# Kernel optimization log

Hardware: AMD Instinct MI355X
Metric: run time of the kernel (lower is better)

The kernel has to match this reference:

```python
import jax, jax.numpy as jnp
import numpy as np

N = 50000
E = 800000
TEXT_VOCAB = 7000
ACTION_DIM = 64
MAX_POS = 5120
POS_DIM = 128   # edge encoder out_dim
NODE_DIM = 128  # text_out 64 + type_out 64
EDGE_DIM = 128
H1 = 256
OUT = 32
NEG_SLOPE = 0.2


def _pos_table():
    # sinusoidal table, [MAX_POS+1, POS_DIM]; even cols = cos, odd cols = sin
    positions = np.arange(0, MAX_POS + 1, dtype=np.float32)
    inv_freq = 1.0 / (10000.0 ** (np.arange(0.0, POS_DIM, 2.0, dtype=np.float32) / POS_DIM))
    si = np.outer(positions, inv_freq)
    tab = np.zeros((MAX_POS + 1, POS_DIM), dtype=np.float32)
    tab[:, 1::2] = np.sin(si)
    tab[:, 0::2] = np.cos(si)
    return jnp.asarray(tab)


def setup_inputs() -> dict:
    key = jax.random.key(0)
    ks = jax.random.split(key, 32)
    ri = jax.random.randint
    nrm = lambda k, s, scale=0.05: (jax.random.normal(k, s, dtype=jnp.float32) * scale)
    x = jnp.stack([ri(ks[0], (N,), 0, TEXT_VOCAB + 1, dtype=jnp.int32),
                   ri(ks[1], (N,), 0, 3, dtype=jnp.int32)], axis=-1)
    edge_index = ri(ks[2], (2, E), 0, N, dtype=jnp.int32)
    edge_attr = jnp.stack([ri(ks[3], (E,), 0, 3, dtype=jnp.int32),
                           ri(ks[4], (E,), 0, MAX_POS + 1, dtype=jnp.int32)], axis=-1)
    d = {
        "x": x, "edge_index": edge_index, "edge_attr": edge_attr,
        "text_emb": nrm(ks[5], (TEXT_VOCAB + 1, 64), 1.0),
        "type_emb": nrm(ks[6], (3, 64), 1.0),
        "flow_emb": nrm(ks[7], (3, EDGE_DIM), 1.0),
        "pos_table": _pos_table(),
        "pos_W": nrm(ks[8], (POS_DIM, POS_DIM)), "pos_b": nrm(ks[9], (POS_DIM,)),
        "c1_Wl": nrm(ks[10], (NODE_DIM, H1)), "c1_bl": nrm(ks[11], (H1,)),
        "c1_Wr": nrm(ks[12], (NODE_DIM, H1)), "c1_br": nrm(ks[13], (H1,)),
        "c1_We": nrm(ks[14], (EDGE_DIM, H1)), "c1_att": nrm(ks[15], (H1,)),
        "c1_bias": nrm(ks[16], (H1,)),
        "c2_Wl": nrm(ks[17], (H1, OUT)), "c2_bl": nrm(ks[18], (OUT,)),
        "c2_Wr": nrm(ks[19], (H1, OUT)), "c2_br": nrm(ks[20], (OUT,)),
        "c2_We": nrm(ks[21], (EDGE_DIM, OUT)), "c2_att": nrm(ks[22], (OUT,)),
        "c2_bias": nrm(ks[23], (OUT,)),
        "policy_W": nrm(ks[24], (OUT, ACTION_DIM), 0.2), "policy_b": nrm(ks[25], (ACTION_DIM,)),
    }
    return d


def gatv2(h, src, dst, ea, Wl, bl, Wr, br, We, att, bias, n):
    # PyG GATv2Conv, heads=1, add_self_loops=True, fill_value='mean'
    loop_attr = jnp.broadcast_to(ea.mean(0), (n, ea.shape[1]))
    s = jnp.concatenate([src, jnp.arange(n, dtype=src.dtype)])
    d = jnp.concatenate([dst, jnp.arange(n, dtype=dst.dtype)])
    ea_full = jnp.concatenate([ea, loop_attr], axis=0)
    xl = h @ Wl + bl  # messages (source side)
    xr = h @ Wr + br  # destination side
    m = xl[s] + xr[d] + ea_full @ We          # [E+n, F]
    e = jnp.where(m > 0, m, NEG_SLOPE * m) @ att  # per-edge logit [E+n]
    emax = jax.ops.segment_max(e, d, num_segments=n)
    a = jnp.exp(e - emax[d])
    denom = jax.ops.segment_sum(a, d, num_segments=n)
    alpha = a / denom[d]
    return jax.ops.segment_sum(alpha[:, None] * xl[s], d, num_segments=n) + bias


def reference(x, edge_index, edge_attr, text_emb, type_emb, flow_emb, pos_table,
              pos_W, pos_b,
              c1_Wl, c1_bl, c1_Wr, c1_br, c1_We, c1_att, c1_bias,
              c2_Wl, c2_bl, c2_Wr, c2_br, c2_We, c2_att, c2_bias,
              policy_W, policy_b):
    # NodeEncoder: concat of text and type embeddings -> [N, 128]
    h = jnp.concatenate([text_emb[x[:, 0]], type_emb[x[:, 1]]], axis=-1)
    # EdgeEncoder: flow embedding + linear(position sinusoid embedding)
    pos = edge_attr[:, 1]
    pos = jnp.where(pos > MAX_POS, pos, MAX_POS)  # faithful to original .where usage
    pos = jnp.clip(pos, 0, MAX_POS)
    ea = flow_emb[edge_attr[:, 0]] + (pos_table[pos] @ pos_W + pos_b)  # [E, 128]
    src, dst = edge_index[0], edge_index[1]
    h = gatv2(h, src, dst, ea, c1_Wl, c1_bl, c1_Wr, c1_br, c1_We, c1_att, c1_bias, h.shape[0])
    h = gatv2(h, src, dst, ea, c2_Wl, c2_bl, c2_Wr, c2_br, c2_We, c2_att, c2_bias, h.shape[0])
    g = h.mean(0)  # [32] graph readout
    logits = g @ policy_W + policy_b
    return jax.nn.softmax(logits, axis=-1)
```

## Files before the change

kernel.cpp:

```cpp
#include <hip/hip_runtime.h>

typedef __attribute__((ext_vector_type(8))) short bf16x8;
typedef __attribute__((ext_vector_type(4))) float f32x4;
typedef __attribute__((ext_vector_type(2))) float f32x2;

#define L2E 1.4426950408889634f
#define S6A (0.6f * L2E)

static __device__ __forceinline__ float wsum64(float v) {
#pragma unroll
    for (int off = 32; off >= 1; off >>= 1) v += __shfl_xor(v, off, 64);
    return v;
}
static __device__ __forceinline__ float wmax64(float v) {
#pragma unroll
    for (int off = 32; off >= 1; off >>= 1) v = fmaxf(v, __shfl_xor(v, off, 64));
    return v;
}

static __device__ __forceinline__ unsigned short bf16r(float a) {
    unsigned int u = __float_as_uint(a);
    return (unsigned short)((u + 0x7FFFu + ((u >> 16) & 1u)) >> 16);
}
static __device__ __forceinline__ unsigned int bf16pack(float a, float b) {
    unsigned int ua = __float_as_uint(a);
    ua = (ua + 0x7FFFu + ((ua >> 16) & 1u)) >> 16;
    unsigned int ub = __float_as_uint(b);
    ub = (ub + 0x7FFFu + ((ub >> 16) & 1u)) & 0xFFFF0000u;
    return ua | ub;
}
static __device__ __forceinline__ float4 bf16x4_to_f4(uint2 u) {
    float4 v;
    v.x = __uint_as_float(u.x << 16);
    v.y = __uint_as_float(u.x & 0xFFFF0000u);
    v.z = __uint_as_float(u.y << 16);
    v.w = __uint_as_float(u.y & 0xFFFF0000u);
    return v;
}
static __device__ __forceinline__ float rflf(float v) {
    return __int_as_float(__builtin_amdgcn_readfirstlane(__float_as_int(v)));
}

#if __has_builtin(__builtin_amdgcn_cvt_pk_f32_fp8) && __has_builtin(__builtin_amdgcn_cvt_pk_fp8_f32)
static __device__ __forceinline__ float4 fp8x4_to_f4(unsigned int u) {
    f32x2 lo = __builtin_amdgcn_cvt_pk_f32_fp8((int)u, false);
    f32x2 hi = __builtin_amdgcn_cvt_pk_f32_fp8((int)u, true);
    return make_float4(lo.x, lo.y, hi.x, hi.y);
}
static __device__ __forceinline__ unsigned int fp8pack4(float a, float b, float c, float d) {
    int u = 0;
    u = __builtin_amdgcn_cvt_pk_fp8_f32(a, b, u, false);
    u = __builtin_amdgcn_cvt_pk_fp8_f32(c, d, u, true);
    return (unsigned int)u;
}
#else
static __device__ __forceinline__ float fp8_1(unsigned int b) {
    return __uint_as_float(((b & 0x80u) << 24) | ((b & 0x7Fu) << 20)) * 0x1p+120f;
}
static __device__ __forceinline__ float4 fp8x4_to_f4(unsigned int u) {
    return make_float4(fp8_1(u & 255u), fp8_1((u >> 8) & 255u),
                       fp8_1((u >> 16) & 255u), fp8_1(u >> 24));
}
static __device__ __forceinline__ unsigned int fp8enc1(float v) {
    unsigned int s = (__float_as_uint(v) >> 24) & 0x80u;
    float a = fminf(fabsf(v), 448.f);
    unsigned int b;
    if (a < 0.015625f) {
        b = (unsigned int)__float2int_rn(a * 512.f);
    } else {
        unsigned int ua = __float_as_uint(a);
        ua += 0x000FFFFFu + ((ua >> 20) & 1u);
        unsigned int e = ua >> 23;
        if (e > 135u) b = 0x7Eu;
        else b = ((e - 120u) << 3) | ((ua >> 20) & 7u);
    }
    return s | b;
}
static __device__ __forceinline__ unsigned int fp8pack4(float a, float b, float c, float d) {
    return fp8enc1(a) | (fp8enc1(b) << 8) | (fp8enc1(c) << 16) | (fp8enc1(d) << 24);
}
#endif

static __device__ __forceinline__ float adot4(const float4 xs, const float4 pre,
                                              const float4 av4) {
    float m0 = xs.x + pre.x, m1 = xs.y + pre.y;
    float m2 = xs.z + pre.z, m3 = xs.w + pre.w;
    float q = av4.x * fabsf(m0);
    q = fmaf(av4.y, fabsf(m1), q);
    q = fmaf(av4.z, fabsf(m2), q);
    q = fmaf(av4.w, fabsf(m3), q);
    return q;
}

static __device__ __forceinline__ int permS(int j) {
    int nb = j >> 7, r = j & 127;
    return nb * 128 + (r & 15) * 8 + (r >> 4);
}
static __device__ __forceinline__ int permK(int s) {
    int nb = s >> 7, r = s & 127;
    return nb * 128 + (r & 7) * 16 + (r >> 3);
}

__global__ void k_edges(const int* __restrict__ ei, const int* __restrict__ ea,
                        int* __restrict__ cntF, int* __restrict__ cnt3, int E) {
    __shared__ int sh3[3];
    if (threadIdx.x < 3) sh3[threadIdx.x] = 0;
    __syncthreads();
    int e = blockIdx.x * blockDim.x + threadIdx.x;
    if (e < E) {
        int dd = ei[E + e];
        int f = ((const int2*)ea)[e].x;
        f = f < 0 ? 0 : (f > 2 ? 2 : f);
        atomicAdd(&cntF[dd * 3 + f], 1);
        atomicAdd(&sh3[f], 1);
    }
    __syncthreads();
    if (threadIdx.x < 3) atomicAdd(&cnt3[threadIdx.x], sh3[threadIdx.x]);
}

__global__ void k_prep_all(const float* __restrict__ pos_table, const float* __restrict__ pos_W,
                           const float* __restrict__ pos_b, const float* __restrict__ flow_emb,
                           const float* __restrict__ We1, const float* __restrict__ We2,
                           const float* __restrict__ att1, const float* __restrict__ bias1,
                           const int* __restrict__ cnt3,
                           float* __restrict__ eaW1p, float* __restrict__ loopW1p,
                           float* __restrict__ att1p, float* __restrict__ bias1p,
                           float* __restrict__ eaW2, float* __restrict__ loopW2,
                           float* __restrict__ delta,
                           const float* __restrict__ Wl1, const float* __restrict__ Wr1,
                           const float* __restrict__ Wl2, const float* __restrict__ Wr2,
                           unsigned short* __restrict__ Bt1, unsigned short* __restrict__ Bt2,
                           int E) {
    __shared__ float posc[128];
    __shared__ float lv[128];
    __shared__ float red4[1024];
    if (blockIdx.x != 0) {
        int i = (blockIdx.x - 1) * 256 + threadIdx.x;
        if (i < 512 * 128) {
            int nn = i >> 7, k = i & 127;
            float v = (nn < 256) ? Wl1[(size_t)k * 256 + nn] : Wr1[(size_t)k * 256 + nn - 256];
            Bt1[i] = bf16r(v);
        } else {
            int j = i - 512 * 128;
            if (j < 64 * 256) {
                int nn = j >> 8, s = j & 255;
                int kk = permK(s);
                float v = (nn < 32) ? Wl2[(size_t)kk * 32 + nn] : Wr2[(size_t)kk * 32 + nn - 32];
                Bt2[j] = bf16r(v);
            }
        }
        return;
    }
    int t = threadIdx.x;
    if (t < 128) {
        const float* row = pos_table + 5120 * 128;
        float a = pos_b[t];
        for (int k = 0; k < 128; ++k) a += row[k] * pos_W[k * 128 + t];
        posc[t] = a;
        float invE = 1.0f / (float)E;
        lv[t] = ((float)cnt3[0] * flow_emb[t] + (float)cnt3[1] * flow_emb[128 + t] +
                 (float)cnt3[2] * flow_emb[256 + t]) * invE + a;
    }
    __syncthreads();
    {
        int j = t;
        float a0 = 0.f, a1 = 0.f, a2 = 0.f, al = 0.f;
        for (int k = 0; k < 128; ++k) {
            float w = We1[k * 256 + j];
            float pc = posc[k];
            a0 += (flow_emb[k] + pc) * w;
            a1 += (flow_emb[128 + k] + pc) * w;
            a2 += (flow_emb[256 + k] + pc) * w;
            al += lv[k] * w;
        }
        int s = permS(j);
        eaW1p[s] = a0; eaW1p[256 + s] = a1; eaW1p[512 + s] = a2; loopW1p[s] = al;
        att1p[s] = att1[j];
        bias1p[s] = bias1[j];
        float avj = att1[j];
        red4[t] = avj * a0;
        red4[256 + t] = avj * a1;
        red4[512 + t] = avj * a2;
        red4[768 + t] = avj * al;
    }
    __syncthreads();
    if (t < 4) {
        float s = 0.f;
        const float* rr = red4 + t * 256;
        for (int k = 0; k < 256; ++k) s += rr[k];
        delta[t] = s * S6A;
    }
    if (t < 32) {
        int j = t;
        float a0 = 0.f, a1 = 0.f, a2 = 0.f, al = 0.f;
        for (int k = 0; k < 128; ++k) {
            float w = We2[k * 32 + j];
            float pc = posc[k];
            a0 += (flow_emb[k] + pc) * w;
            a1 += (flow_emb[128 + k] + pc) * w;
            a2 += (flow_emb[256 + k] + pc) * w;
            al += lv[k] * w;
        }
        eaW2[j] = a0; eaW2[32 + j] = a1; eaW2[64 + j] = a2; loopW2[j] = al;
    }
}

__global__ __launch_bounds__(256) void k_scan_block(const int* __restrict__ cnt,
                                                    int* __restrict__ rowptr,
                                                    int* __restrict__ bsum, int n) {
    __shared__ int sh[256];
    int b = blockIdx.x, t = threadIdx.x;
    int base = b * 1024 + t * 4;
    int v0 = base + 0 < n ? cnt[base + 0] : 0;
    int v1 = base + 1 < n ? cnt[base + 1] : 0;
    int v2 = base + 2 < n ? cnt[base + 2] : 0;
    int v3 = base + 3 < n ? cnt[base + 3] : 0;
    int tot = v0 + v1 + v2 + v3;
    sh[t] = tot;
    __syncthreads();
    for (int off = 1; off < 256; off <<= 1) {
        int x = (t >= off) ? sh[t - off] : 0;
        __syncthreads();
        sh[t] += x;
        __syncthreads();
    }
    int excl = (t > 0) ? sh[t - 1] : 0;
    if (base + 0 < n) rowptr[base + 0] = excl;
    if (base + 1 < n) rowptr[base + 1] = excl + v0;
    if (base + 2 < n) rowptr[base + 2] = excl + v0 + v1;
    if (base + 3 < n) rowptr[base + 3] = excl + v0 + v1 + v2;
    if (t == 255) bsum[b] = sh[255];
}

__global__ __launch_bounds__(256) void k_scan_add(int* __restrict__ rowptr,
        const int* __restrict__ bsum, int* __restrict__ wptr, int n, int nb) {
    __shared__ int red[256];
    int b = blockIdx.x, t = threadIdx.x;
    int lim = b >> 2;
    int local = 0;
    for (int k = t; k < lim; k += 256) local += bsum[k];
    red[t] = local;
    __syncthreads();
    for (int s = 128; s > 0; s >>= 1) {
        if (t < s) red[t] += red[t + s];
        __syncthreads();
    }
    int P = red[0];
    if (b == 0) {
        P = 0;
        int tot = 0;
        for (int k = t; k < nb; k += 256) tot += bsum[k];
        __syncthreads();
        red[t] = tot;
        __syncthreads();
        for (int s = 128; s > 0; s >>= 1) {
            if (t < s) red[t] += red[t + s];
            __syncthreads();
        }
        if (t == 0) rowptr[n] = red[0];
    }
    int i = b * 256 + t;
    if (i < n) {
        int v = rowptr[i] + P;
        rowptr[i] = v;
        wptr[i] = v;
    }
}

__global__ void k_scatter(const int* __restrict__ ei, const int* __restrict__ ea,
                          int* __restrict__ wptr, int* __restrict__ packed, int E) {
    int e = blockIdx.x * blockDim.x + threadIdx.x;
    if (e >= E) return;
    int s = ei[e], dd = ei[E + e];
    int f = ((const int2*)ea)[e].x;
    f = f < 0 ? 0 : (f > 2 ? 2 : f);
    int p = atomicAdd(&wptr[dd * 3 + f], 1);
    packed[p] = s | (f << 16);
}

__global__ __launch_bounds__(256) void k_gemm1(const int* __restrict__ x,
        const float* __restrict__ text_emb, const float* __restrict__ type_emb,
        const unsigned short* __restrict__ Bt,
        const float* __restrict__ bl, const float* __restrict__ br,
        const float* __restrict__ att, float* __restrict__ alpha,
        unsigned char* __restrict__ xl8, unsigned short* __restrict__ xrp, int n) {
    __shared__ unsigned short Ash[64][136];
    __shared__ unsigned short Bsh[128][136];
    int t = threadIdx.x;
    int node0 = blockIdx.x * 64;
    for (int i = t; i < 64 * 128; i += 256) {
        int r = i >> 7, cc = i & 127;
        int nd = node0 + r;
        float v = 0.f;
        if (nd < n)
            v = (cc < 64) ? text_emb[(size_t)x[nd * 2] * 64 + cc]
                          : type_emb[(size_t)x[nd * 2 + 1] * 64 + (cc - 64)];
        Ash[r][cc] = bf16r(v);
    }
    int wave = t >> 6, lane = t & 63;
    int m = lane & 15, q = lane >> 4;
    for (int nb = 0; nb < 4; ++nb) {
        __syncthreads();
        for (int i = t; i < 128 * 16; i += 256) {
            int r = i >> 4, cs = i & 15;
            uint4 v = ((const uint4*)(Bt + (size_t)(nb * 128 + r) * 128))[cs];
            *(uint4*)&Bsh[r][cs * 8] = v;
        }
        __syncthreads();
        f32x4 acc[8];
#pragma unroll
        for (int nt = 0; nt < 8; ++nt) acc[nt] = (f32x4){0.f, 0.f, 0.f, 0.f};
#pragma unroll
        for (int k = 0; k < 128; k += 32) {
            bf16x8 a = *(const bf16x8*)&Ash[wave * 16 + m][k + q * 8];
#pragma unroll
            for (int nt = 0; nt < 8; ++nt) {
                bf16x8 b = *(const bf16x8*)&Bsh[nt * 16 + m][k + q * 8];
                acc[nt] = __builtin_amdgcn_mfma_f32_16x16x32_bf16(a, b, acc[nt], 0, 0, 0);
            }
        }
        float bv[8];
#pragma unroll
// ... 83 lines not shown
#pragma unroll
        for (int nt = 0; nt < 2; ++nt) {
            bf16x8 b = *(const bf16x8*)&Bsh[nh + nt * 16 + m][k + q * 8];
            acc[nt] = __builtin_amdgcn_mfma_f32_16x16x32_bf16(a, b, acc[nt], 0, 0, 0);
        }
    }
#pragma unroll
    for (int r = 0; r < 4; ++r) {
        int node = node0 + mrow + q * 4 + r;
        if (node < n) {
#pragma unroll
            for (int nt = 0; nt < 2; ++nt) {
                int ng = nh + nt * 16 + m;
                float bvv = (ng < 32) ? bl[ng] : br[ng - 32];
                xc[(size_t)node * 64 + ng] = bf16r(acc[nt][r] + bvv);
            }
        }
    }
}

__global__ __launch_bounds__(256) void k_gat256(const unsigned char* __restrict__ xl8,
        const unsigned short* __restrict__ xrp,
        const int* __restrict__ rowptrF, const int* __restrict__ packed,
        const float* __restrict__ eaWp, const float* __restrict__ loopWp,
        const float* __restrict__ attp, const float* __restrict__ biasp,
        const float* __restrict__ alpha, const float* __restrict__ delta,
        unsigned short* __restrict__ h2b, int n) {
    int wid = (blockIdx.x * blockDim.x + threadIdx.x) >> 6;
    if (wid >= n) return;
    int d = __builtin_amdgcn_readfirstlane(wid);
    int lane = threadIdx.x & 63;
    int c = lane * 4;
    const float S4 = 0.4f * L2E;
    float4 xld = fp8x4_to_f4(*(const unsigned int*)(xl8 + (size_t)d * 256 + c));
    float4 xrd = bf16x4_to_f4(((const uint2*)(xrp + (size_t)d * 256))[lane]);
    float4 av = *(const float4*)(attp + c);
    float4 av4;
    av4.x = S4 * av.x; av4.y = S4 * av.y; av4.z = S4 * av.z; av4.w = S4 * av.w;
    float gq = av.x * xrd.x;
    gq = fmaf(av.y, xrd.y, gq); gq = fmaf(av.z, xrd.z, gq); gq = fmaf(av.w, xrd.w, gq);
    float gd = rflf(wsum64(gq) * S6A);
    float ab0 = gd + delta[0], ab1 = gd + delta[1], ab2 = gd + delta[2];
    float ab3 = gd + delta[3];
    float alphad = alpha[d];
    float4 r0 = *(const float4*)(eaWp + c);
    float4 r1 = *(const float4*)(eaWp + 256 + c);
    float4 r2 = *(const float4*)(eaWp + 512 + c);
    float4 lwp = *(const float4*)(loopWp + c);
    r0.x += xrd.x; r0.y += xrd.y; r0.z += xrd.z; r0.w += xrd.w;
    r1.x += xrd.x; r1.y += xrd.y; r1.z += xrd.z; r1.w += xrd.w;
    r2.x += xrd.x; r2.y += xrd.y; r2.z += xrd.z; r2.w += xrd.w;
    lwp.x += xrd.x; lwp.y += xrd.y; lwp.z += xrd.z; lwp.w += xrd.w;
    int jj = lane & 15;
    int a0i = jj << 2, a1i = (jj + 16) << 2, a2i = (jj + 32) << 2, a3i = (jj + 48) << 2;
    bool bq0 = (lane & 16) != 0, bq1 = (lane & 32) != 0;
    float den;
    float4 acc;
    {
        float q = wsum64(adot4(xld, lwp, av4)) + alphad + ab3;
        float wself = exp2f(q);
        den = wself;
        acc.x = wself * xld.x; acc.y = wself * xld.y;
        acc.z = wself * xld.z; acc.w = wself * xld.w;
    }
    int p = rowptrF[d * 3], p1 = rowptrF[d * 3 + 3];
    for (; p + 4 <= p1; p += 4) {
        int pk0 = packed[p],     pk1 = packed[p + 1];
        int pk2 = packed[p + 2], pk3 = packed[p + 3];
        int s0 = pk0 & 0xFFFF, s1 = pk1 & 0xFFFF;
        int s2 = pk2 & 0xFFFF, s3 = pk3 & 0xFFFF;
        int f0 = pk0 >> 16, f1 = pk1 >> 16, f2 = pk2 >> 16, f3 = pk3 >> 16;
        unsigned int g0 = *(const unsigned int*)(xl8 + (size_t)s0 * 256 + c);
        unsigned int g1 = *(const unsigned int*)(xl8 + (size_t)s1 * 256 + c);
        unsigned int g2 = *(const unsigned int*)(xl8 + (size_t)s2 * 256 + c);
        unsigned int g3 = *(const unsigned int*)(xl8 + (size_t)s3 * 256 + c);
        float sc0 = alpha[s0] + ((f0 == 0) ? ab0 : ((f0 == 1) ? ab1 : ab2));
        float sc1 = alpha[s1] + ((f1 == 0) ? ab0 : ((f1 == 1) ? ab1 : ab2));
        float sc2 = alpha[s2] + ((f2 == 0) ? ab0 : ((f2 == 1) ? ab1 : ab2));
        float sc3 = alpha[s3] + ((f3 == 0) ? ab0 : ((f3 == 1) ? ab1 : ab2));
        float4 xs0 = fp8x4_to_f4(g0);
        float4 xs1 = fp8x4_to_f4(g1);
        float4 xs2 = fp8x4_to_f4(g2);
        float4 xs3 = fp8x4_to_f4(g3);
        float q0, q1, q2, q3;
        if (f0 == f3) {
            float4 pr = (f0 == 0) ? r0 : ((f0 == 1) ? r1 : r2);
            q0 = adot4(xs0, pr, av4);
            q1 = adot4(xs1, pr, av4);
            q2 = adot4(xs2, pr, av4);
            q3 = adot4(xs3, pr, av4);
        } else {
            float4 pr0 = (f0 == 0) ? r0 : ((f0 == 1) ? r1 : r2);
            float4 pr1 = (f1 == 0) ? r0 : ((f1 == 1) ? r1 : r2);
            float4 pr2 = (f2 == 0) ? r0 : ((f2 == 1) ? r1 : r2);
            float4 pr3 = (f3 == 0) ? r0 : ((f3 == 1) ? r1 : r2);
            q0 = adot4(xs0, pr0, av4);
            q1 = adot4(xs1, pr1, av4);
            q2 = adot4(xs2, pr2, av4);
            q3 = adot4(xs3, pr3, av4);
        }
        q0 += __shfl_xor(q0, 16, 64); q1 += __shfl_xor(q1, 16, 64);
        q2 += __shfl_xor(q2, 16, 64); q3 += __shfl_xor(q3, 16, 64);
        q0 += __shfl_xor(q0, 32, 64); q1 += __shfl_xor(q1, 32, 64);
        q2 += __shfl_xor(q2, 32, 64); q3 += __shfl_xor(q3, 32, 64);
        float r01 = bq0 ? q1 : q0, r23 = bq0 ? q3 : q2;
        float rr = bq1 ? r23 : r01;
        rr += __shfl_xor(rr, 1, 64); rr += __shfl_xor(rr, 2, 64);
        rr += __shfl_xor(rr, 4, 64); rr += __shfl_xor(rr, 8, 64);
        float s01 = bq0 ? sc1 : sc0, s23 = bq0 ? sc3 : sc2;
        float scv = bq1 ? s23 : s01;
        float w = exp2f(rr + scv);
        int wi = __float_as_int(w);
        float w0 = __int_as_float(__builtin_amdgcn_ds_bpermute(a0i, wi));
        float w1 = __int_as_float(__builtin_amdgcn_ds_bpermute(a1i, wi));
        float w2 = __int_as_float(__builtin_amdgcn_ds_bpermute(a2i, wi));
        float w3 = __int_as_float(__builtin_amdgcn_ds_bpermute(a3i, wi));
        den += (w0 + w1) + (w2 + w3);
        acc.x += w0 * xs0.x + w1 * xs1.x + w2 * xs2.x + w3 * xs3.x;
        acc.y += w0 * xs0.y + w1 * xs1.y + w2 * xs2.y + w3 * xs3.y;
        acc.z += w0 * xs0.z + w1 * xs1.z + w2 * xs2.z + w3 * xs3.z;
        acc.w += w0 * xs0.w + w1 * xs1.w + w2 * xs2.w + w3 * xs3.w;
    }
    for (; p < p1; ++p) {
        int pk = packed[p];
        int s = pk & 0xFFFF, f = pk >> 16;
        unsigned int g = *(const unsigned int*)(xl8 + (size_t)s * 256 + c);
        float sc = alpha[s] + ((f == 0) ? ab0 : ((f == 1) ? ab1 : ab2));
        float4 xs = fp8x4_to_f4(g);
        float4 pr = (f == 0) ? r0 : ((f == 1) ? r1 : r2);
        float q = wsum64(adot4(xs, pr, av4)) + sc;
        float w = exp2f(q);
        den += w;
        acc.x += w * xs.x; acc.y += w * xs.y; acc.z += w * xs.z; acc.w += w * xs.w;
    }
    float inv = 1.f / den;
    float4 bvv = *(const float4*)(biasp + c);
    float ox = fmaf(acc.x, inv, bvv.x), oy = fmaf(acc.y, inv, bvv.y);
    float oz = fmaf(acc.z, inv, bvv.z), ow = fmaf(acc.w, inv, bvv.w);
    ((uint2*)(h2b + (size_t)d * 256))[lane] = make_uint2(bf16pack(ox, oy), bf16pack(oz, ow));
}

__global__ __launch_bounds__(256) void k_gat32(const unsigned short* __restrict__ xc2,
        const int* __restrict__ rowptrF, const int* __restrict__ packed,
        const float* __restrict__ eaW, const float* __restrict__ loopW,
        const float* __restrict__ att, const float* __restrict__ bias,
        float* __restrict__ out, int n) {
    int wid = (blockIdx.x * blockDim.x + threadIdx.x) >> 6;
    if (wid >= n) return;
    int d = __builtin_amdgcn_readfirstlane(wid);
    int lane = threadIdx.x & 63;
    int g = lane >> 4, li = lane & 15;
    unsigned int uxl = ((const unsigned int*)(xc2 + (size_t)d * 64))[li];
    unsigned int uxr = ((const unsigned int*)(xc2 + (size_t)d * 64 + 32))[li];
    float xl0 = __uint_as_float(uxl << 16), xl1 = __uint_as_float(uxl & 0xFFFF0000u);
    float xr0 = __uint_as_float(uxr << 16), xr1 = __uint_as_float(uxr & 0xFFFF0000u);
    float2 avv = ((const float2*)att)[li];
    float a60 = 0.6f * L2E * avv.x, a61 = 0.6f * L2E * avv.y;
    float a40 = 0.4f * L2E * avv.x, a41 = 0.4f * L2E * avv.y;
    float2 e0 = ((const float2*)eaW)[li];
    float2 e1 = ((const float2*)(eaW + 32))[li];
    float2 e2 = ((const float2*)(eaW + 64))[li];
    float p00 = e0.x + xr0, p01 = e0.y + xr1;
    float p10 = e1.x + xr0, p11 = e1.y + xr1;
    float p20 = e2.x + xr0, p21 = e2.y + xr1;
    float den, acc0, acc1;
    {
        float2 lwv = ((const float2*)loopW)[li];
        float m0 = xl0 + xr0 + lwv.x, m1 = xl1 + xr1 + lwv.y;
        float q = a60 * m0 + a40 * fabsf(m0);
        q = fmaf(a61, m1, q); q = fmaf(a41, fabsf(m1), q);
        q += __shfl_xor(q, 1, 64); q += __shfl_xor(q, 2, 64);
        q += __shfl_xor(q, 4, 64); q += __shfl_xor(q, 8, 64);
// ... 19 lines not shown
        float prC0 = (fC == 0) ? p00 : ((fC == 1) ? p10 : p20);
        float prC1 = (fC == 0) ? p01 : ((fC == 1) ? p11 : p21);
        float prD0 = (fD == 0) ? p00 : ((fD == 1) ? p10 : p20);
        float prD1 = (fD == 0) ? p01 : ((fD == 1) ? p11 : p21);
        float xa0 = __uint_as_float(ua << 16), xa1 = __uint_as_float(ua & 0xFFFF0000u);
        float xb0 = __uint_as_float(ub << 16), xb1 = __uint_as_float(ub & 0xFFFF0000u);
        float xcc0 = __uint_as_float(uc << 16), xcc1 = __uint_as_float(uc & 0xFFFF0000u);
        float xd0 = __uint_as_float(ud << 16), xd1 = __uint_as_float(ud & 0xFFFF0000u);
        float ma0 = xa0 + prA0, ma1 = xa1 + prA1;
        float mb0 = xb0 + prB0, mb1 = xb1 + prB1;
        float mc0 = xcc0 + prC0, mc1 = xcc1 + prC1;
        float md0 = xd0 + prD0, md1 = xd1 + prD1;
        float qa = a60 * ma0 + a40 * fabsf(ma0);
        qa = fmaf(a61, ma1, qa); qa = fmaf(a41, fabsf(ma1), qa);
        float qb = a60 * mb0 + a40 * fabsf(mb0);
        qb = fmaf(a61, mb1, qb); qb = fmaf(a41, fabsf(mb1), qb);
        float qc = a60 * mc0 + a40 * fabsf(mc0);
        qc = fmaf(a61, mc1, qc); qc = fmaf(a41, fabsf(mc1), qc);
        float qd = a60 * md0 + a40 * fabsf(md0);
        qd = fmaf(a61, md1, qd); qd = fmaf(a41, fabsf(md1), qd);
#pragma unroll
        for (int off = 1; off <= 8; off <<= 1) {
            qa += __shfl_xor(qa, off, 64);
            qb += __shfl_xor(qb, off, 64);
            qc += __shfl_xor(qc, off, 64);
            qd += __shfl_xor(qd, off, 64);
        }
        float wa = exp2f(qa), wb = exp2f(qb);
        float wc = exp2f(qc), wd = exp2f(qd);
        den += (wa + wb) + (wc + wd);
        acc0 += wa * xa0 + wb * xb0 + wc * xcc0 + wd * xd0;
        acc1 += wa * xa1 + wb * xb1 + wc * xcc1 + wd * xd1;
    }
    for (; p < pB; p += 4) {
        int pk = packed[p];
        unsigned int u = ((const unsigned int*)(xc2 + (size_t)(pk & 0xFFFF) * 64))[li];
        int f = pk >> 16;
        float pre0 = (f == 0) ? p00 : ((f == 1) ? p10 : p20);
        float pre1 = (f == 0) ? p01 : ((f == 1) ? p11 : p21);
        float x0 = __uint_as_float(u << 16), x1 = __uint_as_float(u & 0xFFFF0000u);
        float m0 = x0 + pre0, m1 = x1 + pre1;
        float q = a60 * m0 + a40 * fabsf(m0);
        q = fmaf(a61, m1, q); q = fmaf(a41, fabsf(m1), q);
        q += __shfl_xor(q, 1, 64); q += __shfl_xor(q, 2, 64);
        q += __shfl_xor(q, 4, 64); q += __shfl_xor(q, 8, 64);
        float w = exp2f(q);
        den += w;
        acc0 = fmaf(w, x0, acc0);
        acc1 = fmaf(w, x1, acc1);
    }
    acc0 += __shfl_xor(acc0, 16, 64); acc0 += __shfl_xor(acc0, 32, 64);
    acc1 += __shfl_xor(acc1, 16, 64); acc1 += __shfl_xor(acc1, 32, 64);
    den  += __shfl_xor(den, 16, 64);  den  += __shfl_xor(den, 32, 64);
    if (g == 0) {
        float2 bvv = ((const float2*)bias)[li];
        float inv = 1.f / den;
        float2 o;
        o.x = fmaf(acc0, inv, bvv.x);
        o.y = fmaf(acc1, inv, bvv.y);
        ((float2*)(out + (size_t)d * 32))[li] = o;
    }
}

__global__ __launch_bounds__(256) void k_tail(const float* __restrict__ out2,
        float* __restrict__ gsum, int* __restrict__ done,
        const float* __restrict__ policy_W, const float* __restrict__ policy_b,
// ... 69 lines not shown
    const int E = in_sizes[1] / 2;
    const int n3 = 3 * N;

    char* base = (char*)d_ws;
    size_t off = 0;
    auto alloc = [&](size_t bytes) -> void* {
        void* p = base + off;
        off = (off + bytes + 255) & ~(size_t)255;
        return p;
    };
    unsigned char*  xl8  = (unsigned char*)alloc((size_t)N * 256);
    unsigned short* xrp  = (unsigned short*)alloc((size_t)N * 256 * 2);
    unsigned short* h2b  = (unsigned short*)alloc((size_t)N * 256 * 2);
    unsigned short* xc2  = (unsigned short*)alloc((size_t)N * 64 * 2);
    float*          out2 = (float*)alloc((size_t)N * 32 * 4);
    unsigned short* Bt1  = (unsigned short*)alloc((size_t)512 * 128 * 2);
    unsigned short* Bt2  = (unsigned short*)alloc((size_t)64 * 256 * 2);
    int*            zreg   = (int*)alloc((size_t)(n3 + 40 + N) * 4);
    int*            cntF   = zreg;
    int*            cnt3   = zreg + n3;
    float*          gsum   = (float*)(zreg + n3 + 4);
    int*            done   = zreg + n3 + 36;
    float*          alpha1 = (float*)(zreg + n3 + 40);
    int*            rowptrF= (int*)alloc((size_t)(n3 + 1) * 4);
    int*            packed = (int*)alloc((size_t)E * 4);
    int*            bsum   = (int*)alloc(256 * 4);
    float*          delta1 = (float*)alloc(4 * 4);
    float*          eaW1p  = (float*)alloc(768 * 4);
    float*          loopW1p= (float*)alloc(256 * 4);
    float*          att1p  = (float*)alloc(256 * 4);
    float*          bias1p = (float*)alloc(256 * 4);
    float*          eaW2   = (float*)alloc(96 * 4);
    float*          loopW2 = (float*)alloc(32 * 4);

    hipMemsetAsync(zreg, 0, (size_t)(n3 + 40 + N) * 4, stream);

    k_edges<<<(E + 255) / 256, 256, 0, stream>>>(edge_index, edge_attr, cntF, cnt3, E);
    k_prep_all<<<1 + (512 * 128 + 64 * 256) / 256, 256, 0, stream>>>(
        pos_table, pos_W, pos_b, flow_emb, c1_We, c2_We, c1_att, c1_bias, cnt3,
        eaW1p, loopW1p, att1p, bias1p, eaW2, loopW2, delta1,
        c1_Wl, c1_Wr, c2_Wl, c2_Wr, Bt1, Bt2, E);

    int nb = (n3 + 1023) / 1024;
    k_scan_block<<<nb, 256, 0, stream>>>(cntF, rowptrF, bsum, n3);
    k_scan_add<<<(n3 + 255) / 256, 256, 0, stream>>>(rowptrF, bsum, cntF, n3, nb);
    k_scatter<<<(E + 255) / 256, 256, 0, stream>>>(edge_index, edge_attr, cntF, packed, E);

    k_gemm1<<<(N + 63) / 64, 256, 0, stream>>>(x, text_emb, type_emb, Bt1,
                                               c1_bl, c1_br, c1_att, alpha1, xl8, xrp, N);
    k_gat256<<<(N + 3) / 4, 256, 0, stream>>>(xl8, xrp, rowptrF, packed, eaW1p, loopW1p,
                                              att1p, bias1p, alpha1, delta1, h2b, N);

    k_gemm2<<<(N + 31) / 32, 256, 0, stream>>>(h2b, Bt2, c2_bl, c2_br, xc2, N);
    k_gat32<<<(N + 3) / 4, 256, 0, stream>>>(xc2, rowptrF, packed, eaW2, loopW2,
                                             c2_att, c2_bias, out2, N);

    k_tail<<<256, 256, 0, stream>>>(out2, gsum, done, policy_W, policy_b, out, N);
}
```

Measured before the change: 411.3 us.

## Merge setup kernels, use packed f32x2 math in GAT256, unroll GAT32 tail

Merges the edge-count and weight-prep kernels into one launch. The self-loop precompute moves into an extra block of the scan kernel, and the scatter is fused with the first GEMM as independent block ranges. Together these cut launch count and let independent work overlap. The 256-wide GAT aggregation is rewritten with two-float vectors so the compiler can emit packed FP32 ops, and the 32-wide GAT gains a two-edge remainder loop. The fused kernels keep the bulky GEMM blocks, and their shared-memory footprint, in the same launch as the lightweight scatter blocks.

New measurement: 394.0 us. 1.04x faster.

```diff
diff --git a/kernel.cpp b/kernel.cpp
--- a/kernel.cpp
+++ b/kernel.cpp
@@ -29,23 +29,17 @@
     ub = (ub + 0x7FFFu + ((ub >> 16) & 1u)) & 0xFFFF0000u;
     return ua | ub;
 }
-static __device__ __forceinline__ float4 bf16x4_to_f4(uint2 u) {
-    float4 v;
-    v.x = __uint_as_float(u.x << 16);
-    v.y = __uint_as_float(u.x & 0xFFFF0000u);
-    v.z = __uint_as_float(u.y << 16);
-    v.w = __uint_as_float(u.y & 0xFFFF0000u);
-    return v;
-}
 static __device__ __forceinline__ float rflf(float v) {
     return __int_as_float(__builtin_amdgcn_readfirstlane(__float_as_int(v)));
 }
+static __device__ __forceinline__ f32x2 sp2(float v) {
+    f32x2 r; r.x = v; r.y = v; return r;
+}
 
 #if __has_builtin(__builtin_amdgcn_cvt_pk_f32_fp8) && __has_builtin(__builtin_amdgcn_cvt_pk_fp8_f32)
-static __device__ __forceinline__ float4 fp8x4_to_f4(unsigned int u) {
-    f32x2 lo = __builtin_amdgcn_cvt_pk_f32_fp8((int)u, false);
-    f32x2 hi = __builtin_amdgcn_cvt_pk_f32_fp8((int)u, true);
-    return make_float4(lo.x, lo.y, hi.x, hi.y);
+static __device__ __forceinline__ void fp8dec(unsigned int u, f32x2& lo, f32x2& hi) {
+    lo = __builtin_amdgcn_cvt_pk_f32_fp8((int)u, false);
+    hi = __builtin_amdgcn_cvt_pk_f32_fp8((int)u, true);
 }
 static __device__ __forceinline__ unsigned int fp8pack4(float a, float b, float c, float d) {
     int u = 0;
@@ -57,9 +51,9 @@
 static __device__ __forceinline__ float fp8_1(unsigned int b) {
     return __uint_as_float(((b & 0x80u) << 24) | ((b & 0x7Fu) << 20)) * 0x1p+120f;
 }
-static __device__ __forceinline__ float4 fp8x4_to_f4(unsigned int u) {
-    return make_float4(fp8_1(u & 255u), fp8_1((u >> 8) & 255u),
-                       fp8_1((u >> 16) & 255u), fp8_1(u >> 24));
+static __device__ __forceinline__ void fp8dec(unsigned int u, f32x2& lo, f32x2& hi) {
+    lo.x = fp8_1(u & 255u); lo.y = fp8_1((u >> 8) & 255u);
+    hi.x = fp8_1((u >> 16) & 255u); hi.y = fp8_1(u >> 24);
 }
 static __device__ __forceinline__ unsigned int fp8enc1(float v) {
     unsigned int s = (__float_as_uint(v) >> 24) & 0x80u;
@@ -81,15 +75,14 @@
 }
 #endif
 
-static __device__ __forceinline__ float adot4(const float4 xs, const float4 pre,
-                                              const float4 av4) {
-    float m0 = xs.x + pre.x, m1 = xs.y + pre.y;
-    float m2 = xs.z + pre.z, m3 = xs.w + pre.w;
-    float q = av4.x * fabsf(m0);
-    q = fmaf(av4.y, fabsf(m1), q);
-    q = fmaf(av4.z, fabsf(m2), q);
-    q = fmaf(av4.w, fabsf(m3), q);
-    return q;
+static __device__ __forceinline__ float adot_pk(f32x2 xlo, f32x2 xhi, f32x2 plo, f32x2 phi,
+                                                f32x2 alo, f32x2 ahi) {
+    f32x2 mlo = xlo + plo;
+    f32x2 mhi = xhi + phi;
+    mlo = __builtin_elementwise_max(mlo, -mlo);
+    mhi = __builtin_elementwise_max(mhi, -mhi);
+    f32x2 qp = mlo * alo + mhi * ahi;
+    return qp.x + qp.y;
 }
 
 static __device__ __forceinline__ int permS(int j) {
@@ -101,41 +94,38 @@
     return nb * 128 + (r & 7) * 16 + (r >> 3);
 }
 
-__global__ void k_edges(const int* __restrict__ ei, const int* __restrict__ ea,
-                        int* __restrict__ cntF, int* __restrict__ cnt3, int E) {
+__global__ void k_edges_prep(const int* __restrict__ ei, const int* __restrict__ ea,
+        int* __restrict__ cntF, int* __restrict__ cnt3, int E, int EB,
+        const float* __restrict__ pos_table, const float* __restrict__ pos_W,
+        const float* __restrict__ pos_b, const float* __restrict__ flow_emb,
+        const float* __restrict__ We1, const float* __restrict__ We2,
+        const float* __restrict__ att1, const float* __restrict__ bias1,
+        float* __restrict__ eaW1p, float* __restrict__ att1p, float* __restrict__ bias1p,
+        float* __restrict__ eaW2, float* __restrict__ delta, float* __restrict__ poscS,
+        const float* __restrict__ Wl1, const float* __restrict__ Wr1,
+        const float* __restrict__ Wl2, const float* __restrict__ Wr2,
+        unsigned short* __restrict__ Bt1, unsigned short* __restrict__ Bt2) {
     __shared__ int sh3[3];
-    if (threadIdx.x < 3) sh3[threadIdx.x] = 0;
-    __syncthreads();
-    int e = blockIdx.x * blockDim.x + threadIdx.x;
-    if (e < E) {
-        int dd = ei[E + e];
-        int f = ((const int2*)ea)[e].x;
-        f = f < 0 ? 0 : (f > 2 ? 2 : f);
-        atomicAdd(&cntF[dd * 3 + f], 1);
-        atomicAdd(&sh3[f], 1);
-    }
-    __syncthreads();
-    if (threadIdx.x < 3) atomicAdd(&cnt3[threadIdx.x], sh3[threadIdx.x]);
-}
-
-__global__ void k_prep_all(const float* __restrict__ pos_table, const float* __restrict__ pos_W,
-                           const float* __restrict__ pos_b, const float* __restrict__ flow_emb,
-                           const float* __restrict__ We1, const float* __restrict__ We2,
-                           const float* __restrict__ att1, const float* __restrict__ bias1,
-                           const int* __restrict__ cnt3,
-                           float* __restrict__ eaW1p, float* __restrict__ loopW1p,
-                           float* __restrict__ att1p, float* __restrict__ bias1p,
-                           float* __restrict__ eaW2, float* __restrict__ loopW2,
-                           float* __restrict__ delta,
-                           const float* __restrict__ Wl1, const float* __restrict__ Wr1,
-                           const float* __restrict__ Wl2, const float* __restrict__ Wr2,
-                           unsigned short* __restrict__ Bt1, unsigned short* __restrict__ Bt2,
-                           int E) {
     __shared__ float posc[128];
-    __shared__ float lv[128];
-    __shared__ float red4[1024];
-    if (blockIdx.x != 0) {
-        int i = (blockIdx.x - 1) * 256 + threadIdx.x;
+    __shared__ float red4[768];
+    int bid = blockIdx.x, t = threadIdx.x;
+    if (bid < EB) {
+        if (t < 3) sh3[t] = 0;
+        __syncthreads();
+        int e = bid * 256 + t;
+        if (e < E) {
+            int dd = ei[E + e];
+            int f = ((const int2*)ea)[e].x;
+            f = f < 0 ? 0 : (f > 2 ? 2 : f);
+            atomicAdd(&cntF[dd * 3 + f], 1);
+            atomicAdd(&sh3[f], 1);
+        }
+        __syncthreads();
+        if (t < 3) atomicAdd(&cnt3[t], sh3[t]);
+        return;
+    }
+    if (bid < EB + 320) {
+        int i = (bid - EB) * 256 + t;
         if (i < 512 * 128) {
             int nn = i >> 7, k = i & 127;
             float v = (nn < 256) ? Wl1[(size_t)k * 256 + nn] : Wr1[(size_t)k * 256 + nn - 256];
@@ -151,40 +141,33 @@
         }
         return;
     }
-    int t = threadIdx.x;
     if (t < 128) {
         const float* row = pos_table + 5120 * 128;
         float a = pos_b[t];
         for (int k = 0; k < 128; ++k) a += row[k] * pos_W[k * 128 + t];
         posc[t] = a;
-        float invE = 1.0f / (float)E;
-        lv[t] = ((float)cnt3[0] * flow_emb[t] + (float)cnt3[1] * flow_emb[128 + t] +
-                 (float)cnt3[2] * flow_emb[256 + t]) * invE + a;
+        poscS[t] = a;
     }
     __syncthreads();
     {
         int j = t;
-        float a0 = 0.f, a1 = 0.f, a2 = 0.f, al = 0.f;
+        float a0 = 0.f, a1 = 0.f, a2 = 0.f;
         for (int k = 0; k < 128; ++k) {
             float w = We1[k * 256 + j];
             float pc = posc[k];
             a0 += (flow_emb[k] + pc) * w;
             a1 += (flow_emb[128 + k] + pc) * w;
             a2 += (flow_emb[256 + k] + pc) * w;
-            al += lv[k] * w;
         }
         int s = permS(j);
-        eaW1p[s] = a0; eaW1p[256 + s] = a1; eaW1p[512 + s] = a2; loopW1p[s] = al;
+        eaW1p[s] = a0; eaW1p[256 + s] = a1; eaW1p[512 + s] = a2;
         att1p[s] = att1[j];
         bias1p[s] = bias1[j];
         float avj = att1[j];
-        red4[t] = avj * a0;
-        red4[256 + t] = avj * a1;
-        red4[512 + t] = avj * a2;
-        red4[768 + t] = avj * al;
+        red4[t] = avj * a0; red4[256 + t] = avj * a1; red4[512 + t] = avj * a2;
     }
     __syncthreads();
-    if (t < 4) {
+    if (t < 3) {
         float s = 0.f;
         const float* rr = red4 + t * 256;
         for (int k = 0; k < 256; ++k) s += rr[k];
@@ -192,24 +175,56 @@
     }
     if (t < 32) {
         int j = t;
-        float a0 = 0.f, a1 = 0.f, a2 = 0.f, al = 0.f;
+        float a0 = 0.f, a1 = 0.f, a2 = 0.f;
         for (int k = 0; k < 128; ++k) {
             float w = We2[k * 32 + j];
             float pc = posc[k];
             a0 += (flow_emb[k] + pc) * w;
             a1 += (flow_emb[128 + k] + pc) * w;
             a2 += (flow_emb[256 + k] + pc) * w;
-            al += lv[k] * w;
-        }
-        eaW2[j] = a0; eaW2[32 + j] = a1; eaW2[64 + j] = a2; loopW2[j] = al;
+        }
+        eaW2[j] = a0; eaW2[32 + j] = a1; eaW2[64 + j] = a2;
     }
 }
 
 __global__ __launch_bounds__(256) void k_scan_block(const int* __restrict__ cnt,
-                                                    int* __restrict__ rowptr,
-                                                    int* __restrict__ bsum, int n) {
+        int* __restrict__ rowptr, int* __restrict__ bsum, int n, int nb,
+        const int* __restrict__ cnt3, const float* __restrict__ poscS,
+        const float* __restrict__ flow_emb, const float* __restrict__ We1,
+        const float* __restrict__ We2, const float* __restrict__ att1,
+        float* __restrict__ loopW1p, float* __restrict__ loopW2,
+        float* __restrict__ delta, int E) {
     __shared__ int sh[256];
+    __shared__ float lv[128];
+    __shared__ float red[256];
     int b = blockIdx.x, t = threadIdx.x;
+    if (b == nb) {
+        if (t < 128) {
+            float invE = 1.0f / (float)E;
+            lv[t] = ((float)cnt3[0] * flow_emb[t] + (float)cnt3[1] * flow_emb[128 + t] +
+                     (float)cnt3[2] * flow_emb[256 + t]) * invE + poscS[t];
+        }
+        __syncthreads();
+        {
+            int j = t;
+            float al = 0.f;
+            for (int k = 0; k < 128; ++k) al += lv[k] * We1[k * 256 + j];
+            loopW1p[permS(j)] = al;
+            red[t] = att1[j] * al;
+        }
+        __syncthreads();
+        if (t == 0) {
+            float s = 0.f;
+            for (int k = 0; k < 256; ++k) s += red[k];
+            delta[3] = s * S6A;
+        }
+        if (t < 32) {
+            float al = 0.f;
+            for (int k = 0; k < 128; ++k) al += lv[k] * We2[k * 32 + t];
+            loopW2[t] = al;
+        }
+        return;
+    }
     int base = b * 1024 + t * 4;
     int v0 = base + 0 < n ? cnt[base + 0] : 0;
     int v1 = base + 1 < n ? cnt[base + 1] : 0;
@@ -267,18 +282,10 @@
     }
 }
 
-__global__ void k_scatter(const int* __restrict__ ei, const int* __restrict__ ea,
-                          int* __restrict__ wptr, int* __restrict__ packed, int E) {
-    int e = blockIdx.x * blockDim.x + threadIdx.x;
-    if (e >= E) return;
-    int s = ei[e], dd = ei[E + e];
-    int f = ((const int2*)ea)[e].x;
-    f = f < 0 ? 0 : (f > 2 ? 2 : f);
-    int p = atomicAdd(&wptr[dd * 3 + f], 1);
-    packed[p] = s | (f << 16);
-}
-
-__global__ __launch_bounds__(256) void k_gemm1(const int* __restrict__ x,
+__global__ __launch_bounds__(256) void k_scatter_gemm1(
+        const int* __restrict__ ei, const int* __restrict__ ea,
+        int* __restrict__ wptr, int* __restrict__ packed, int E, int SB,
+        const int* __restrict__ x,
         const float* __restrict__ text_emb, const float* __restrict__ type_emb,
         const unsigned short* __restrict__ Bt,
         const float* __restrict__ bl, const float* __restrict__ br,
@@ -287,7 +294,17 @@
     __shared__ unsigned short Ash[64][136];
     __shared__ unsigned short Bsh[128][136];
     int t = threadIdx.x;
-    int node0 = blockIdx.x * 64;
+    if ((int)blockIdx.x < SB) {
+        int e = blockIdx.x * 256 + t;
+        if (e >= E) return;
+        int s = ei[e], dd = ei[E + e];
+        int f = ((const int2*)ea)[e].x;
+        f = f < 0 ? 0 : (f > 2 ? 2 : f);
+        int p = atomicAdd(&wptr[dd * 3 + f], 1);
+        packed[p] = s | (f << 16);
+        return;
+    }
+    int node0 = (blockIdx.x - SB) * 64;
     for (int i = t; i < 64 * 128; i += 256) {
         int r = i >> 7, cc = i & 127;
         int nd = node0 + r;
@@ -437,36 +454,38 @@
     int lane = threadIdx.x & 63;
     int c = lane * 4;
     const float S4 = 0.4f * L2E;
-    float4 xld = fp8x4_to_f4(*(const unsigned int*)(xl8 + (size_t)d * 256 + c));
-    float4 xrd = bf16x4_to_f4(((const uint2*)(xrp + (size_t)d * 256))[lane]);
-    float4 av = *(const float4*)(attp + c);
-    float4 av4;
-    av4.x = S4 * av.x; av4.y = S4 * av.y; av4.z = S4 * av.z; av4.w = S4 * av.w;
-    float gq = av.x * xrd.x;
-    gq = fmaf(av.y, xrd.y, gq); gq = fmaf(av.z, xrd.z, gq); gq = fmaf(av.w, xrd.w, gq);
-    float gd = rflf(wsum64(gq) * S6A);
+    f32x2 xldL, xldH;
+    fp8dec(*(const unsigned int*)(xl8 + (size_t)d * 256 + c), xldL, xldH);
+    uint2 uxr = ((const uint2*)(xrp + (size_t)d * 256))[lane];
+    f32x2 xrdL, xrdH;
+    xrdL.x = __uint_as_float(uxr.x << 16); xrdL.y = __uint_as_float(uxr.x & 0xFFFF0000u);
+    xrdH.x = __uint_as_float(uxr.y << 16); xrdH.y = __uint_as_float(uxr.y & 0xFFFF0000u);
+    f32x2 avL = *(const f32x2*)(attp + c), avH = *(const f32x2*)(attp + c + 2);
+    f32x2 a4L = avL * sp2(S4), a4H = avH * sp2(S4);
+    f32x2 gp = avL * xrdL + avH * xrdH;
+    float gd = rflf(wsum64(gp.x + gp.y) * S6A);
     float ab0 = gd + delta[0], ab1 = gd + delta[1], ab2 = gd + delta[2];
     float ab3 = gd + delta[3];
     float alphad = alpha[d];
-    float4 r0 = *(const float4*)(eaWp + c);
-    float4 r1 = *(const float4*)(eaWp + 256 + c);
-    float4 r2 = *(const float4*)(eaWp + 512 + c);
-    float4 lwp = *(const float4*)(loopWp + c);
-    r0.x += xrd.x; r0.y += xrd.y; r0.z += xrd.z; r0.w += xrd.w;
-    r1.x += xrd.x; r1.y += xrd.y; r1.z += xrd.z; r1.w += xrd.w;
-    r2.x += xrd.x; r2.y += xrd.y; r2.z += xrd.z; r2.w += xrd.w;
-    lwp.x += xrd.x; lwp.y += xrd.y; lwp.z += xrd.z; lwp.w += xrd.w;
+    f32x2 r0L = *(const f32x2*)(eaWp + c) + xrdL;
+    f32x2 r0H = *(const f32x2*)(eaWp + c + 2) + xrdH;
+    f32x2 r1L = *(const f32x2*)(eaWp + 256 + c) + xrdL;
+    f32x2 r1H = *(const f32x2*)(eaWp + 256 + c + 2) + xrdH;
+    f32x2 r2L = *(const f32x2*)(eaWp + 512 + c) + xrdL;
+    f32x2 r2H = *(const f32x2*)(eaWp + 512 + c + 2) + xrdH;
+    f32x2 lwL = *(const f32x2*)(loopWp + c) + xrdL;
+    f32x2 lwH = *(const f32x2*)(loopWp + c + 2) + xrdH;
     int jj = lane & 15;
     int a0i = jj << 2, a1i = (jj + 16) << 2, a2i = (jj + 32) << 2, a3i = (jj + 48) << 2;
     bool bq0 = (lane & 16) != 0, bq1 = (lane & 32) != 0;
     float den;
-    float4 acc;
+    f32x2 accL, accH;
     {
-        float q = wsum64(adot4(xld, lwp, av4)) + alphad + ab3;
+        float q = wsum64(adot_pk(xldL, xldH, lwL, lwH, a4L, a4H)) + alphad + ab3;
         float wself = exp2f(q);
         den = wself;
-        acc.x = wself * xld.x; acc.y = wself * xld.y;
-        acc.z = wself * xld.z; acc.w = wself * xld.w;
+        accL = xldL * sp2(wself);
+        accH = xldH * sp2(wself);
     }
     int p = rowptrF[d * 3], p1 = rowptrF[d * 3 + 3];
     for (; p + 4 <= p1; p += 4) {
@@ -483,26 +502,30 @@
         float sc1 = alpha[s1] + ((f1 == 0) ? ab0 : ((f1 == 1) ? ab1 : ab2));
         float sc2 = alpha[s2] + ((f2 == 0) ? ab0 : ((f2 == 1) ? ab1 : ab2));
         float sc3 = alpha[s3] + ((f3 == 0) ? ab0 : ((f3 == 1) ? ab1 : ab2));
-        float4 xs0 = fp8x4_to_f4(g0);
-        float4 xs1 = fp8x4_to_f4(g1);
-        float4 xs2 = fp8x4_to_f4(g2);
-        float4 xs3 = fp8x4_to_f4(g3);
+        f32x2 x0L, x0H, x1L, x1H, x2L, x2H, x3L, x3H;
+        fp8dec(g0, x0L, x0H); fp8dec(g1, x1L, x1H);
+        fp8dec(g2, x2L, x2H); fp8dec(g3, x3L, x3H);
         float q0, q1, q2, q3;
         if (f0 == f3) {
-            float4 pr = (f0 == 0) ? r0 : ((f0 == 1) ? r1 : r2);
-            q0 = adot4(xs0, pr, av4);
-            q1 = adot4(xs1, pr, av4);
-            q2 = adot4(xs2, pr, av4);
-            q3 = adot4(xs3, pr, av4);
+            f32x2 pL = (f0 == 0) ? r0L : ((f0 == 1) ? r1L : r2L);
+            f32x2 pH = (f0 == 0) ? r0H : ((f0 == 1) ? r1H : r2H);
+            q0 = adot_pk(x0L, x0H, pL, pH, a4L, a4H);
+            q1 = adot_pk(x1L, x1H, pL, pH, a4L, a4H);
+            q2 = adot_pk(x2L, x2H, pL, pH, a4L, a4H);
+            q3 = adot_pk(x3L, x3H, pL, pH, a4L, a4H);
         } else {
-            float4 pr0 = (f0 == 0) ? r0 : ((f0 == 1) ? r1 : r2);
-            float4 pr1 = (f1 == 0) ? r0 : ((f1 == 1) ? r1 : r2);
-            float4 pr2 = (f2 == 0) ? r0 : ((f2 == 1) ? r1 : r2);
-            float4 pr3 = (f3 == 0) ? r0 : ((f3 == 1) ? r1 : r2);
-            q0 = adot4(xs0, pr0, av4);
-            q1 = adot4(xs1, pr1, av4);
-            q2 = adot4(xs2, pr2, av4);
-            q3 = adot4(xs3, pr3, av4);
+            f32x2 p0L = (f0 == 0) ? r0L : ((f0 == 1) ? r1L : r2L);
+            f32x2 p0H = (f0 == 0) ? r0H : ((f0 == 1) ? r1H : r2H);
+            f32x2 p1L_ = (f1 == 0) ? r0L : ((f1 == 1) ? r1L : r2L);
+            f32x2 p1H_ = (f1 == 0) ? r0H : ((f1 == 1) ? r1H : r2H);
+            f32x2 p2L = (f2 == 0) ? r0L : ((f2 == 1) ? r1L : r2L);
+            f32x2 p2H = (f2 == 0) ? r0H : ((f2 == 1) ? r1H : r2H);
+            f32x2 p3L = (f3 == 0) ? r0L : ((f3 == 1) ? r1L : r2L);
+            f32x2 p3H = (f3 == 0) ? r0H : ((f3 == 1) ? r1H : r2H);
+            q0 = adot_pk(x0L, x0H, p0L, p0H, a4L, a4H);
+            q1 = adot_pk(x1L, x1H, p1L_, p1H_, a4L, a4H);
+            q2 = adot_pk(x2L, x2H, p2L, p2H, a4L, a4H);
+            q3 = adot_pk(x3L, x3H, p3L, p3H, a4L, a4H);
         }
         q0 += __shfl_xor(q0, 16, 64); q1 += __shfl_xor(q1, 16, 64);
         q2 += __shfl_xor(q2, 16, 64); q3 += __shfl_xor(q3, 16, 64);
@@ -521,28 +544,30 @@
         float w2 = __int_as_float(__builtin_amdgcn_ds_bpermute(a2i, wi));
         float w3 = __int_as_float(__builtin_amdgcn_ds_bpermute(a3i, wi));
         den += (w0 + w1) + (w2 + w3);
-        acc.x += w0 * xs0.x + w1 * xs1.x + w2 * xs2.x + w3 * xs3.x;
-        acc.y += w0 * xs0.y + w1 * xs1.y + w2 * xs2.y + w3 * xs3.y;
-        acc.z += w0 * xs0.z + w1 * xs1.z + w2 * xs2.z + w3 * xs3.z;
-        acc.w += w0 * xs0.w + w1 * xs1.w + w2 * xs2.w + w3 * xs3.w;
+        accL += x0L * sp2(w0) + x1L * sp2(w1) + x2L * sp2(w2) + x3L * sp2(w3);
+        accH += x0H * sp2(w0) + x1H * sp2(w1) + x2H * sp2(w2) + x3H * sp2(w3);
     }
     for (; p < p1; ++p) {
         int pk = packed[p];
         int s = pk & 0xFFFF, f = pk >> 16;
         unsigned int g = *(const unsigned int*)(xl8 + (size_t)s * 256 + c);
         float sc = alpha[s] + ((f == 0) ? ab0 : ((f == 1) ? ab1 : ab2));
-        float4 xs = fp8x4_to_f4(g);
-        float4 pr = (f == 0) ? r0 : ((f == 1) ? r1 : r2);
-        float q = wsum64(adot4(xs, pr, av4)) + sc;
+        f32x2 xL, xH;
+        fp8dec(g, xL, xH);
+        f32x2 pL = (f == 0) ? r0L : ((f == 1) ? r1L : r2L);
+        f32x2 pH = (f == 0) ? r0H : ((f == 1) ? r1H : r2H);
+        float q = wsum64(adot_pk(xL, xH, pL, pH, a4L, a4H)) + sc;
         float w = exp2f(q);
         den += w;
-        acc.x += w * xs.x; acc.y += w * xs.y; acc.z += w * xs.z; acc.w += w * xs.w;
+        accL += xL * sp2(w);
+        accH += xH * sp2(w);
     }
     float inv = 1.f / den;
-    float4 bvv = *(const float4*)(biasp + c);
-    float ox = fmaf(acc.x, inv, bvv.x), oy = fmaf(acc.y, inv, bvv.y);
-    float oz = fmaf(acc.z, inv, bvv.z), ow = fmaf(acc.w, inv, bvv.w);
-    ((uint2*)(h2b + (size_t)d * 256))[lane] = make_uint2(bf16pack(ox, oy), bf16pack(oz, ow));
+    f32x2 bvL = *(const f32x2*)(biasp + c), bvH = *(const f32x2*)(biasp + c + 2);
+    f32x2 oL = accL * sp2(inv) + bvL;
+    f32x2 oH = accH * sp2(inv) + bvH;
+    ((uint2*)(h2b + (size_t)d * 256))[lane] =
+        make_uint2(bf16pack(oL.x, oL.y), bf16pack(oH.x, oH.y));
 }
 
 __global__ __launch_bounds__(256) void k_gat32(const unsigned short* __restrict__ xc2,
@@ -628,6 +653,33 @@
         acc0 += wa * xa0 + wb * xb0 + wc * xcc0 + wd * xd0;
         acc1 += wa * xa1 + wb * xb1 + wc * xcc1 + wd * xd1;
     }
+    for (; p + 4 < pB; p += 8) {
+        int pkA = packed[p], pkB = packed[p + 4];
+        unsigned int ua = ((const unsigned int*)(xc2 + (size_t)(pkA & 0xFFFF) * 64))[li];
+        unsigned int ub = ((const unsigned int*)(xc2 + (size_t)(pkB & 0xFFFF) * 64))[li];
+        int fA = pkA >> 16, fB = pkB >> 16;
+        float prA0 = (fA == 0) ? p00 : ((fA == 1) ? p10 : p20);
+        float prA1 = (fA == 0) ? p01 : ((fA == 1) ? p11 : p21);
+        float prB0 = (fB == 0) ? p00 : ((fB == 1) ? p10 : p20);
+        float prB1 = (fB == 0) ? p01 : ((fB == 1) ? p11 : p21);
+        float xa0 = __uint_as_float(ua << 16), xa1 = __uint_as_float(ua & 0xFFFF0000u);
+        float xb0 = __uint_as_float(ub << 16), xb1 = __uint_as_float(ub & 0xFFFF0000u);
+        float ma0 = xa0 + prA0, ma1 = xa1 + prA1;
+        float mb0 = xb0 + prB0, mb1 = xb1 + prB1;
+        float qa = a60 * ma0 + a40 * fabsf(ma0);
+        qa = fmaf(a61, ma1, qa); qa = fmaf(a41, fabsf(ma1), qa);
+        float qb = a60 * mb0 + a40 * fabsf(mb0);
+        qb = fmaf(a61, mb1, qb); qb = fmaf(a41, fabsf(mb1), qb);
+#pragma unroll
+        for (int off = 1; off <= 8; off <<= 1) {
+            qa += __shfl_xor(qa, off, 64);
+            qb += __shfl_xor(qb, off, 64);
+        }
+        float wa = exp2f(qa), wb = exp2f(qb);
+        den += wa + wb;
+        acc0 += wa * xa0 + wb * xb0;
+        acc1 += wa * xa1 + wb * xb1;
+    }
     for (; p < pB; p += 4) {
         int pk = packed[p];
         unsigned int u = ((const unsigned int*)(xc2 + (size_t)(pk & 0xFFFF) * 64))[li];
@@ -763,26 +815,33 @@
     float*          bias1p = (float*)alloc(256 * 4);
     float*          eaW2   = (float*)alloc(96 * 4);
     float*          loopW2 = (float*)alloc(32 * 4);
+    float*          poscS  = (float*)alloc(128 * 4);
 
     hipMemsetAsync(zreg, 0, (size_t)(n3 + 40 + N) * 4, stream);
 
-    k_edges<<<(E + 255) / 256, 256, 0, stream>>>(edge_index, edge_attr, cntF, cnt3, E);
-    k_prep_all<<<1 + (512 * 128 + 64 * 256) / 256, 256, 0, stream>>>(
-        pos_table, pos_W, pos_b, flow_emb, c1_We, c2_We, c1_att, c1_bias, cnt3,
-        eaW1p, loopW1p, att1p, bias1p, eaW2, loopW2, delta1,
-        c1_Wl, c1_Wr, c2_Wl, c2_Wr, Bt1, Bt2, E);
+    const int EB = (E + 255) / 256;
+    k_edges_prep<<<EB + 320 + 1, 256, 0, stream>>>(
+        edge_index, edge_attr, cntF, cnt3, E, EB,
+        pos_table, pos_W, pos_b, flow_emb, c1_We, c2_We, c1_att, c1_bias,
+        eaW1p, att1p, bias1p, eaW2, delta1, poscS,
+        c1_Wl, c1_Wr, c2_Wl, c2_Wr, Bt1, Bt2);
 
     int nb = (n3 + 1023) / 1024;
-    k_scan_block<<<nb, 256, 0, stream>>>(cntF, rowptrF, bsum, n3);
+    k_scan_block<<<nb + 1, 256, 0, stream>>>(cntF, rowptrF, bsum, n3, nb,
+        cnt3, poscS, flow_emb, c1_We, c2_We, c1_att, loopW1p, loopW2, delta1, E);
+
     k_scan_add<<<(n3 + 255) / 256, 256, 0, stream>>>(rowptrF, bsum, cntF, n3, nb);
-    k_scatter<<<(E + 255) / 256, 256, 0, stream>>>(edge_index, edge_attr, cntF, packed, E);
-
-    k_gemm1<<<(N + 63) / 64, 256, 0, stream>>>(x, text_emb, type_emb, Bt1,
-                                               c1_bl, c1_br, c1_att, alpha1, xl8, xrp, N);
+
+    const int GB = (N + 63) / 64;
+    k_scatter_gemm1<<<EB + GB, 256, 0, stream>>>(
+        edge_index, edge_attr, cntF, packed, E, EB,
+        x, text_emb, type_emb, Bt1, c1_bl, c1_br, c1_att, alpha1, xl8, xrp, N);
+
     k_gat256<<<(N + 3) / 4, 256, 0, stream>>>(xl8, xrp, rowptrF, packed, eaW1p, loopW1p,
                                               att1p, bias1p, alpha1, delta1, h2b, N);
 
     k_gemm2<<<(N + 31) / 32, 256, 0, stream>>>(h2b, Bt2, c2_bl, c2_br, xc2, N);
+
     k_gat32<<<(N + 3) / 4, 256, 0, stream>>>(xc2, rowptrF, packed, eaW2, loopW2,
                                              c2_att, c2_bias, out2, N);
 
```
